# Performance work log

Hardware: AMD Instinct MI355X
Metric: run time of the kernel (lower is better)

## Reference

```python
import jax, jax.numpy as jnp
import numpy as np

B, S, E = 2, 4096, 512

def setup_inputs() -> dict:
    key = jax.random.key(0)
    kx, kq, kk, kv, ko = jax.random.split(key, 5)
    scale = 1.0 / np.sqrt(E)  # init-style scaling for weights
    return {
        "x": jax.random.normal(kx, (B, S, E), dtype=jnp.float32),
        "Wq": jax.random.normal(kq, (E, E), dtype=jnp.float32) * scale,
        "Wk": jax.random.normal(kk, (E, E), dtype=jnp.float32) * scale,
        "Wv": jax.random.normal(kv, (E, E), dtype=jnp.float32) * scale,
        "Wo": jax.random.normal(ko, (E, E), dtype=jnp.float32) * scale,
        "bo": jnp.zeros((E,), dtype=jnp.float32),
    }

def reference(x, Wq, Wk, Wv, Wo, bo):
    # nn.Linear: y = x @ W.T  (weights stored [out, in])
    q = jnp.einsum("bse,fe->bsf", x, Wq)
    k = jnp.einsum("bse,fe->bsf", x, Wk)
    v = jnp.einsum("bse,fe->bsf", x, Wv)
    inv_scale = 1.0 / jnp.sqrt(jnp.asarray(x.shape[-1], x.dtype))
    scores = jnp.einsum("bqe,bke->bqk", q, k) * inv_scale  # [B,S,S]
    S_len = x.shape[1]
    # torch.triu(ones) keeps j >= i; masked_fill where triu==0 masks j < i
    row = jnp.arange(S_len)[:, None]
    col = jnp.arange(S_len)[None, :]
    keep = col >= row  # [S,S], faithfully anti-causal as in the source
    scores = jnp.where(keep[None, :, :], scores, jnp.asarray(-jnp.inf, scores.dtype))
    attn = jax.nn.softmax(scores, axis=-1)
    # dropout p=0.0 -> identity
    out = jnp.einsum("bqk,bke->bqe", attn, v)
    return jnp.einsum("bse,fe->bsf", out, Wo) + bo
```

## Files before the change

kernel.cpp:

```cpp
#include <hip/hip_runtime.h>
#include <hip/hip_bf16.h>

#define S_LEN 4096
#define E_DIM 512
#define B_DIM 2
#define M_ROWS (B_DIM * S_LEN)

typedef __attribute__((ext_vector_type(8))) short short8;
typedef __attribute__((ext_vector_type(4))) float floatx4;

__device__ __forceinline__ unsigned short f2bf(float f) {
    unsigned u = __float_as_uint(f);
    unsigned r = (u + 0x7fffu + ((u >> 16) & 1u)) >> 16;
    return (unsigned short)r;
}
__device__ __forceinline__ float bf2f(unsigned short u) {
    return __uint_as_float((unsigned)u << 16);
}

__device__ __forceinline__ void async_copy16(unsigned short* lds, const unsigned short* g) {
    auto gp = (const __attribute__((address_space(1))) unsigned int*)g;
    auto lp = (__attribute__((address_space(3))) unsigned int*)lds;
    __builtin_amdgcn_global_load_lds(gp, lp, 16, 0, 0);
}

struct MapArg { unsigned short m[576]; };

__global__ __launch_bounds__(256) void convert_bf16(
    const float* __restrict__ x,  const float* __restrict__ wq,
    const float* __restrict__ wk, const float* __restrict__ wv,
    const float* __restrict__ wo, unsigned short* __restrict__ dstU,
    unsigned short* __restrict__ dstWo)
{
    long i = (long)blockIdx.x * 1024 + (long)threadIdx.x * 4;
    const float* src; long off; unsigned short* dst; long doff;
    if      (i < 4194304) { src = x;  off = i;           dst = dstU;  doff = i; }
    else if (i < 4456448) { src = wq; off = i - 4194304; dst = dstU;  doff = i; }
    else if (i < 4718592) { src = wk; off = i - 4456448; dst = dstU;  doff = i; }
    else if (i < 4980736) { src = wv; off = i - 4718592; dst = dstU;  doff = i; }
    else                  { src = wo; off = i - 4980736; dst = dstWo; doff = i - 4980736; }
    float4 v = *(const float4*)(src + off);
    ushort4 o;
    o.x = f2bf(v.x); o.y = f2bf(v.y); o.z = f2bf(v.z); o.w = f2bf(v.w);
    *(ushort4*)(dst + doff) = o;
}

__device__ __forceinline__ void gemm_core(
    const unsigned short* __restrict__ A, const unsigned short* __restrict__ W,
    void* __restrict__ Cv, const float* __restrict__ bias, int mode,
    int m0, int n0)
{
    __shared__ unsigned short As[128 * 32];
    __shared__ unsigned short Bs[128 * 32];
    const int tid = threadIdx.x;
    const int lane = tid & 63, wave = tid >> 6;
    const int wm = wave >> 1, wn = wave & 1;
    const int q4 = lane >> 4, l16 = lane & 15;

    floatx4 acc[4][4];
#pragma unroll
    for (int i = 0; i < 4; ++i)
#pragma unroll
        for (int j = 0; j < 4; ++j) acc[i][j] = (floatx4){0.f, 0.f, 0.f, 0.f};

    const int srow = lane >> 2;
    const int scol = (lane & 3) * 8;

    for (int k0 = 0; k0 < 512; k0 += 32) {
        async_copy16(&As[(wave * 16) * 32],
                     A + (size_t)(m0 + wave * 16 + srow) * 512 + k0 + scol);
        async_copy16(&As[(64 + wave * 16) * 32],
                     A + (size_t)(m0 + 64 + wave * 16 + srow) * 512 + k0 + scol);
        async_copy16(&Bs[(wave * 16) * 32],
                     W + (size_t)(n0 + wave * 16 + srow) * 512 + k0 + scol);
        async_copy16(&Bs[(64 + wave * 16) * 32],
                     W + (size_t)(n0 + 64 + wave * 16 + srow) * 512 + k0 + scol);
        __syncthreads();
        short8 af[4], bfr[4];
#pragma unroll
        for (int i = 0; i < 4; ++i) {
            af[i]  = *(const short8*)&As[(wm * 64 + i * 16 + l16) * 32 + q4 * 8];
            bfr[i] = *(const short8*)&Bs[(wn * 64 + i * 16 + l16) * 32 + q4 * 8];
        }
#pragma unroll
        for (int i = 0; i < 4; ++i)
#pragma unroll
            for (int j = 0; j < 4; ++j)
                acc[i][j] = __builtin_amdgcn_mfma_f32_16x16x32_bf16(af[i], bfr[j], acc[i][j], 0, 0, 0);
        __syncthreads();
    }

    if (mode == 0) {
        unsigned short* C = (unsigned short*)Cv;
#pragma unroll
        for (int i = 0; i < 4; ++i) {
            int rowb = m0 + wm * 64 + i * 16 + q4 * 4;
#pragma unroll
            for (int j = 0; j < 4; ++j) {
                int col = n0 + wn * 64 + j * 16 + l16;
#pragma unroll
                for (int rg = 0; rg < 4; ++rg)
                    C[(size_t)(rowb + rg) * 512 + col] = f2bf(acc[i][j][rg]);
            }
        }
    } else if (mode == 1) {
        unsigned short* C = (unsigned short*)Cv;
#pragma unroll
        for (int i = 0; i < 4; ++i) {
            int grow = m0 + wm * 64 + i * 16 + q4 * 4;
            int b = grow >> 12, s = grow & 4095;
#pragma unroll
            for (int j = 0; j < 4; ++j) {
                int e = n0 + wn * 64 + j * 16 + l16;
                ushort4 pk;
                pk.x = f2bf(acc[i][j][0]); pk.y = f2bf(acc[i][j][1]);
                pk.z = f2bf(acc[i][j][2]); pk.w = f2bf(acc[i][j][3]);
                *(ushort4*)(C + (size_t)b * 512 * 4096 + (size_t)e * 4096 + s) = pk;
            }
        }
    } else {
        float* C = (float*)Cv;
#pragma unroll
        for (int i = 0; i < 4; ++i) {
            int rowb = m0 + wm * 64 + i * 16 + q4 * 4;
#pragma unroll
            for (int j = 0; j < 4; ++j) {
                int col = n0 + wn * 64 + j * 16 + l16;
                float bv = bias[col];
#pragma unroll
                for (int rg = 0; rg < 4; ++rg)
                    C[(size_t)(rowb + rg) * 512 + col] = acc[i][j][rg] + bv;
            }
        }
    }
}

__global__ __launch_bounds__(256) void gemm_qkv(
    const unsigned short* __restrict__ xb,
    const unsigned short* __restrict__ Wqb, const unsigned short* __restrict__ Wkb,
    const unsigned short* __restrict__ Wvb,
    unsigned short* __restrict__ Qb, unsigned short* __restrict__ Kb,
    unsigned short* __restrict__ Vtb)
{
    const int z = blockIdx.z;
    const unsigned short* W = (z == 0) ? Wqb : (z == 1) ? Wkb : Wvb;
    unsigned short* C = (z == 0) ? Qb : (z == 1) ? Kb : Vtb;
    gemm_core(xb, W, C, nullptr, (z == 2) ? 1 : 0, blockIdx.y * 128, blockIdx.x * 128);
}

__global__ __launch_bounds__(256) void gemm_out(
    const unsigned short* __restrict__ AOb, const unsigned short* __restrict__ Wob,
    const float* __restrict__ bo, float* __restrict__ out)
{
    gemm_core(AOb, Wob, out, bo, 2, blockIdx.y * 128, blockIdx.x * 128);
}

__global__ __launch_bounds__(512, 2) void flash_mfma(
    const unsigned short* __restrict__ Qg, const unsigned short* __restrict__ Kg,
    const unsigned short* __restrict__ Vt,
    unsigned short* __restrict__ Oh, float* __restrict__ Lb, MapArg map)
{
    const int enc = map.m[blockIdx.x];
    const int tile = enc & 63, ch = (enc >> 6) & 7, bb = enc >> 9;
    const int i0 = tile * 64;
    const int lo0 = 512 * ch, hi = lo0 + 512;
    const int lo = (i0 > lo0) ? i0 : lo0;
    const int lo_al = lo & ~127;
    const int nsteps = (hi - lo_al) >> 7;

    const int tid = threadIdx.x;
    const int lane = tid & 63, w = tid >> 6;
    const int q4 = lane >> 4, l16 = lane & 15;
    const int e = l16 & 7;
    const float scale = 0.044194173824159216f;
    const float MREF = 4.0f;

    __shared__ unsigned short Qs[64 * 512];
    __shared__ unsigned short Plds[2][64][136];
    __shared__ float Lred[8][64];

    const size_t rowbase = (size_t)bb * S_LEN;
    const size_t vbase   = (size_t)bb * (size_t)512 * 4096;

#pragma unroll
    for (int rr = 0; rr < 8; ++rr) {
        const int row = w * 8 + rr;
        const unsigned short* src = Qg + (rowbase + i0 + row) * 512
                                    + ((lane ^ (row & 7)) << 3);
        async_copy16(&Qs[row * 512], src);
    }

    floatx4 oacc[4][4];
#pragma unroll
    for (int mg = 0; mg < 4; ++mg)
#pragma unroll
        for (int nc = 0; nc < 4; ++nc) oacc[mg][nc] = (floatx4){0.f, 0.f, 0.f, 0.f};
    float l_acc[4] = {0.f, 0.f, 0.f, 0.f};

    const unsigned short* qb0 = &Qs[l16 * 512 + ((q4 ^ e) << 3)];
    const unsigned short* qb1 = &Qs[l16 * 512 + (((q4 + 4) ^ e) << 3)];
    const unsigned short* kpbase = Kg + (rowbase + 16 * w + l16) * 512 + (q4 << 3);
    const unsigned short* vpbase = Vt + vbase + (size_t)(w * 64 + l16) * 4096 + (q4 << 3);

    short8 kf[16];
    {
        const unsigned short* kp = kpbase + (size_t)lo_al * 512;
#pragma unroll
        for (int ks = 0; ks < 16; ++ks)
            kf[ks] = *(const short8*)(kp + ks * 32);
    }
    short8 vf[4][4];
#pragma unroll
    for (int nc = 0; nc < 4; ++nc) {
        const unsigned short* vpn = vpbase + (size_t)(nc * 16) * 4096 + lo_al;
#pragma unroll
        for (int kslot = 0; kslot < 4; ++kslot)
            vf[nc][kslot] = *(const short8*)(vpn + kslot * 32);
    }

    __syncthreads();

    for (int t = 0; t < nsteps; ++t) {
        const int j0 = lo_al + t * 128;
        const int jp = (t + 1 < nsteps) ? j0 + 128 : j0;
        const int buf = t & 1;

        floatx4 sf[4];
#pragma unroll
        for (int mg = 0; mg < 4; ++mg) sf[mg] = (floatx4){0.f, 0.f, 0.f, 0.f};
        __builtin_amdgcn_s_setprio(1);
#pragma unroll
        for (int ks = 0; ks < 16; ++ks) {
            const unsigned short* qb = (ks & 1) ? qb1 : qb0;
#pragma unroll
            for (int mg = 0; mg < 4; ++mg) {
                short8 a = *(const short8*)(qb + mg * 8192 + (ks >> 1) * 64);
                sf[mg] = __builtin_amdgcn_mfma_f32_16x16x32_bf16(kf[ks], a, sf[mg], 0, 0, 0);
            }
        }
        __builtin_amdgcn_s_setprio(0);

        {
            const unsigned short* kp = kpbase + (size_t)jp * 512;
#pragma unroll
            for (int ks = 0; ks < 16; ++ks)
                kf[ks] = *(const short8*)(kp + ks * 32);
        }

        const int kb = j0 + 16 * w + (q4 << 2);
        const bool full = (j0 >= i0 + 64);
#pragma unroll
        for (int mg = 0; mg < 4; ++mg) {
            const int row = i0 + mg * 16 + l16;
            float p0 = __expf(sf[mg][0] * scale - MREF);
            float p1 = __expf(sf[mg][1] * scale - MREF);
            float p2 = __expf(sf[mg][2] * scale - MREF);
            float p3 = __expf(sf[mg][3] * scale - MREF);
            if (!full) {
                p0 = (kb + 0 >= row) ? p0 : 0.f;
                p1 = (kb + 1 >= row) ? p1 : 0.f;
                p2 = (kb + 2 >= row) ? p2 : 0.f;
                p3 = (kb + 3 >= row) ? p3 : 0.f;
            }
            l_acc[mg] += p0 + p1 + p2 + p3;
            ushort4 pk;
            pk.x = f2bf(p0); pk.y = f2bf(p1); pk.z = f2bf(p2); pk.w = f2bf(p3);
            *(ushort4*)&Plds[buf][mg * 16 + l16][16 * w + (q4 << 2)] = pk;
        }

        asm volatile("s_waitcnt lgkmcnt(0)" ::: "memory");
        __builtin_amdgcn_s_barrier();
        __builtin_amdgcn_sched_barrier(0);

        __builtin_amdgcn_s_setprio(1);
#pragma unroll
        for (int kslot = 0; kslot < 4; ++kslot) {
#pragma unroll
            for (int mg = 0; mg < 4; ++mg) {
                short8 ap = *(const short8*)&Plds[buf][mg * 16 + l16][kslot * 32 + (q4 << 3)];
#pragma unroll
                for (int nc = 0; nc < 4; ++nc)
                    oacc[mg][nc] = __builtin_amdgcn_mfma_f32_16x16x32_bf16(
                        ap, vf[nc][kslot], oacc[mg][nc], 0, 0, 0);
            }
        }
        __builtin_amdgcn_s_setprio(0);

#pragma unroll
        for (int nc = 0; nc < 4; ++nc) {
            const unsigned short* vpn = vpbase + (size_t)(nc * 16) * 4096 + jp;
#pragma unroll
            for (int kslot = 0; kslot < 4; ++kslot)
                vf[nc][kslot] = *(const short8*)(vpn + kslot * 32);
        }
    }

#pragma unroll
    for (int mg = 0; mg < 4; ++mg) {
        float v = l_acc[mg];
        v += __shfl_xor(v, 16, 64);
        v += __shfl_xor(v, 32, 64);
        if (q4 == 0) Lred[w][mg * 16 + l16] = v;
    }
    __syncthreads();

    const int slot = 8 * ch * (ch + 1) + bb * 8 * (ch + 1) + tile;
    if (tid < 64) {
        float sum = 0.f;
#pragma unroll
        for (int ww = 0; ww < 8; ++ww) sum += Lred[ww][tid];
        Lb[(size_t)slot * 64 + tid] = sum;
    }

    unsigned short* Op = Oh + (size_t)slot * 64 * 512;
#pragma unroll
    for (int mg = 0; mg < 4; ++mg)
#pragma unroll
        for (int nc = 0; nc < 4; ++nc)
#pragma unroll
            for (int rg = 0; rg < 4; ++rg)
                Op[(size_t)(mg * 16 + q4 * 4 + rg) * 512 + w * 64 + nc * 16 + l16]
                    = f2bf(oacc[mg][nc][rg]);
}

__global__ __launch_bounds__(256) void flash_merge(
    const unsigned short* __restrict__ Oh, const float* __restrict__ Lb,
    unsigned short* __restrict__ AO)
{
    const int row = blockIdx.x;
    const int c = threadIdx.x * 2;
    const int bb = row >> 12, i = row & 4095;
    const int t = i >> 6, ri = i & 63;
    const int chmin = i >> 9;
    float lsum = 0.f, v0 = 0.f, v1 = 0.f;
    for (int ch = chmin; ch < 8; ++ch) {
        int slot = 8 * ch * (ch + 1) + bb * 8 * (ch + 1) + t;
        lsum += Lb[(size_t)slot * 64 + ri];
        const unsigned short* p = Oh + (size_t)slot * 64 * 512 + (size_t)ri * 512 + c;
        v0 += bf2f(p[0]);
        v1 += bf2f(p[1]);
    }
    float inv = 1.f / lsum;
    ushort2 o; o.x = f2bf(v0 * inv); o.y = f2bf(v1 * inv);
    *(ushort2*)(AO + (size_t)row * 512 + c) = o;
}

static MapArg build_map() {
    MapArg mp{};
    for (int x = 0; x < 8; ++x) {
        const int bb = x >> 2;
        const int chs[2] = {7 - (x & 3), x & 3};
        int enc[72], st[72], n = 0;
        for (int ci = 0; ci < 2; ++ci) {
            const int ch = chs[ci];
            for (int t = 0; t < 8 * (ch + 1); ++t) {
                int i0 = t * 64, lo0 = 512 * ch, hi = lo0 + 512;
                int lo = (i0 > lo0) ? i0 : lo0;
                int lo_al = lo & ~127;
                enc[n] = t | (ch << 6) | (bb << 9);
                st[n] = (hi - lo_al) >> 7;
                ++n;
            }
        }
        for (int i = 1; i < n; ++i) {
            int ev = enc[i], sv = st[i], j = i - 1;
            while (j >= 0 && st[j] < sv) { st[j + 1] = st[j]; enc[j + 1] = enc[j]; --j; }
            st[j + 1] = sv; enc[j + 1] = ev;
        }
        for (int j = 0; j < n; ++j) mp.m[x + 8 * j] = (unsigned short)enc[j];
    }
    return mp;
}

extern "C" void kernel_launch(void* const* d_in, const int* in_sizes, int n_in,
                              void* d_out, int out_size, void* d_ws, size_t ws_size,
                              hipStream_t stream) {
    (void)in_sizes; (void)n_in; (void)out_size; (void)ws_size;
    const float* x  = (const float*)d_in[0];
    const float* Wq = (const float*)d_in[1];
    const float* Wk = (const float*)d_in[2];
    const float* Wv = (const float*)d_in[3];
    const float* Wo = (const float*)d_in[4];
    const float* bo = (const float*)d_in[5];
    float* out = (float*)d_out;

    unsigned short* ws  = (unsigned short*)d_ws;
    unsigned short* Wob = ws;
    unsigned short* QAb = ws + 262144;
    unsigned short* Kb  = QAb + 4194304;
    unsigned short* Vtb = Kb + 4194304;
    unsigned short* U   = Vtb + 4194304;
    unsigned short* xb  = U;
    unsigned short* Wqb = U + 4194304;
    unsigned short* Wkb = Wqb + 262144;
    unsigned short* Wvb = Wkb + 262144;
    unsigned short* Ohb = U;
    float* Lbf = (float*)(U + 18874368);

    static const MapArg mp = build_map();

    convert_bf16<<<5120, 256, 0, stream>>>(x, Wq, Wk, Wv, Wo, U, Wob);

    gemm_qkv<<<dim3(4, 64, 3), 256, 0, stream>>>(xb, Wqb, Wkb, Wvb, QAb, Kb, Vtb);

    flash_mfma<<<576, 512, 0, stream>>>(QAb, Kb, Vtb, Ohb, Lbf, mp);

    flash_merge<<<8192, 256, 0, stream>>>(Ohb, Lbf, QAb);

    gemm_out<<<dim3(4, 64), 256, 0, stream>>>(QAb, Wob, bo, out);
}
```

Baseline: 234.4 us.

## Widen projection GEMM K-tile with XOR swizzle; drop register prefetch in attention loop

The projection GEMM now stages 64-wide K slices in LDS with an XOR-swizzled column layout, which halves the number of barrier pairs and is meant to reduce LDS bank conflicts. In the attention loop, K and V fragments are no longer prefetched into registers one step ahead. They are loaded at the start of each step, and the hand-written waitcnt/barrier is replaced by __syncthreads. This cuts register pressure and may raise occupancy, but global-load latency is no longer hidden behind the previous step's MFMA work.

Measured after the change: 216.0 us. 7.8% less time.

```diff
diff --git a/kernel.cpp b/kernel.cpp
--- a/kernel.cpp
+++ b/kernel.cpp
@@ -50,12 +50,13 @@
     void* __restrict__ Cv, const float* __restrict__ bias, int mode,
     int m0, int n0)
 {
-    __shared__ unsigned short As[128 * 32];
-    __shared__ unsigned short Bs[128 * 32];
+    __shared__ unsigned short As[128 * 64];
+    __shared__ unsigned short Bs[128 * 64];
     const int tid = threadIdx.x;
     const int lane = tid & 63, wave = tid >> 6;
     const int wm = wave >> 1, wn = wave & 1;
     const int q4 = lane >> 4, l16 = lane & 15;
+    const int er = l16 & 7;
 
     floatx4 acc[4][4];
 #pragma unroll
@@ -63,30 +64,38 @@
 #pragma unroll
         for (int j = 0; j < 4; ++j) acc[i][j] = (floatx4){0.f, 0.f, 0.f, 0.f};
 
-    const int srow = lane >> 2;
-    const int scol = (lane & 3) * 8;
-
-    for (int k0 = 0; k0 < 512; k0 += 32) {
-        async_copy16(&As[(wave * 16) * 32],
-                     A + (size_t)(m0 + wave * 16 + srow) * 512 + k0 + scol);
-        async_copy16(&As[(64 + wave * 16) * 32],
-                     A + (size_t)(m0 + 64 + wave * 16 + srow) * 512 + k0 + scol);
-        async_copy16(&Bs[(wave * 16) * 32],
-                     W + (size_t)(n0 + wave * 16 + srow) * 512 + k0 + scol);
-        async_copy16(&Bs[(64 + wave * 16) * 32],
-                     W + (size_t)(n0 + 64 + wave * 16 + srow) * 512 + k0 + scol);
+    const int srow = lane >> 3;
+    const int scol = ((lane & 7) ^ srow) << 3;
+
+    for (int k0 = 0; k0 < 512; k0 += 64) {
+#pragma unroll
+        for (int c = 0; c < 4; ++c) {
+            const int rbase = c * 32 + wave * 8;
+            async_copy16(&As[rbase * 64],
+                         A + (size_t)(m0 + rbase + srow) * 512 + k0 + scol);
+            async_copy16(&Bs[rbase * 64],
+                         W + (size_t)(n0 + rbase + srow) * 512 + k0 + scol);
+        }
         __syncthreads();
-        short8 af[4], bfr[4];
+        short8 af[4][2], bfr[4][2];
+        const int c0 = (q4 ^ er) * 8;
 #pragma unroll
         for (int i = 0; i < 4; ++i) {
-            af[i]  = *(const short8*)&As[(wm * 64 + i * 16 + l16) * 32 + q4 * 8];
-            bfr[i] = *(const short8*)&Bs[(wn * 64 + i * 16 + l16) * 32 + q4 * 8];
-        }
-#pragma unroll
-        for (int i = 0; i < 4; ++i)
-#pragma unroll
-            for (int j = 0; j < 4; ++j)
-                acc[i][j] = __builtin_amdgcn_mfma_f32_16x16x32_bf16(af[i], bfr[j], acc[i][j], 0, 0, 0);
+            const int ra = (wm * 64 + i * 16 + l16) * 64;
+            const int rb = (wn * 64 + i * 16 + l16) * 64;
+            af[i][0]  = *(const short8*)&As[ra + c0];
+            af[i][1]  = *(const short8*)&As[ra + (c0 ^ 32)];
+            bfr[i][0] = *(const short8*)&Bs[rb + c0];
+            bfr[i][1] = *(const short8*)&Bs[rb + (c0 ^ 32)];
+        }
+#pragma unroll
+        for (int h = 0; h < 2; ++h)
+#pragma unroll
+            for (int i = 0; i < 4; ++i)
+#pragma unroll
+                for (int j = 0; j < 4; ++j)
+                    acc[i][j] = __builtin_amdgcn_mfma_f32_16x16x32_bf16(
+                        af[i][h], bfr[j][h], acc[i][j], 0, 0, 0);
         __syncthreads();
     }
 
@@ -200,30 +209,18 @@
     const unsigned short* qb0 = &Qs[l16 * 512 + ((q4 ^ e) << 3)];
     const unsigned short* qb1 = &Qs[l16 * 512 + (((q4 + 4) ^ e) << 3)];
     const unsigned short* kpbase = Kg + (rowbase + 16 * w + l16) * 512 + (q4 << 3);
-    const unsigned short* vpbase = Vt + vbase + (size_t)(w * 64 + l16) * 4096 + (q4 << 3);
-
-    short8 kf[16];
-    {
-        const unsigned short* kp = kpbase + (size_t)lo_al * 512;
+
+    __syncthreads();
+
+    for (int t = 0; t < nsteps; ++t) {
+        const int j0 = lo_al + t * 128;
+        const int buf = t & 1;
+
+        short8 kf[16];
+        const unsigned short* kp = kpbase + (size_t)j0 * 512;
 #pragma unroll
         for (int ks = 0; ks < 16; ++ks)
             kf[ks] = *(const short8*)(kp + ks * 32);
-    }
-    short8 vf[4][4];
-#pragma unroll
-    for (int nc = 0; nc < 4; ++nc) {
-        const unsigned short* vpn = vpbase + (size_t)(nc * 16) * 4096 + lo_al;
-#pragma unroll
-        for (int kslot = 0; kslot < 4; ++kslot)
-            vf[nc][kslot] = *(const short8*)(vpn + kslot * 32);
-    }
-
-    __syncthreads();
-
-    for (int t = 0; t < nsteps; ++t) {
-        const int j0 = lo_al + t * 128;
-        const int jp = (t + 1 < nsteps) ? j0 + 128 : j0;
-        const int buf = t & 1;
 
         floatx4 sf[4];
 #pragma unroll
@@ -240,11 +237,14 @@
         }
         __builtin_amdgcn_s_setprio(0);
 
-        {
-            const unsigned short* kp = kpbase + (size_t)jp * 512;
-#pragma unroll
-            for (int ks = 0; ks < 16; ++ks)
-                kf[ks] = *(const short8*)(kp + ks * 32);
+        short8 vf[4][4];
+#pragma unroll
+        for (int nc = 0; nc < 4; ++nc) {
+            const unsigned short* vpn = Vt + vbase
+                + (size_t)(w * 64 + nc * 16 + l16) * 4096 + j0 + (q4 << 3);
+#pragma unroll
+            for (int kslot = 0; kslot < 4; ++kslot)
+                vf[nc][kslot] = *(const short8*)(vpn + kslot * 32);
         }
 
         const int kb = j0 + 16 * w + (q4 << 2);
@@ -267,10 +267,7 @@
             pk.x = f2bf(p0); pk.y = f2bf(p1); pk.z = f2bf(p2); pk.w = f2bf(p3);
             *(ushort4*)&Plds[buf][mg * 16 + l16][16 * w + (q4 << 2)] = pk;
         }
-
-        asm volatile("s_waitcnt lgkmcnt(0)" ::: "memory");
-        __builtin_amdgcn_s_barrier();
-        __builtin_amdgcn_sched_barrier(0);
+        __syncthreads();
 
         __builtin_amdgcn_s_setprio(1);
 #pragma unroll
@@ -285,14 +282,6 @@
             }
         }
         __builtin_amdgcn_s_setprio(0);
-
-#pragma unroll
-        for (int nc = 0; nc < 4; ++nc) {
-            const unsigned short* vpn = vpbase + (size_t)(nc * 16) * 4096 + jp;
-#pragma unroll
-            for (int kslot = 0; kslot < 4; ++kslot)
-                vf[nc][kslot] = *(const short8*)(vpn + kslot * 32);
-        }
     }
 
 #pragma unroll
```
